# Performance work log

Measured on AMD Instinct MI355X. Metric: run time of the kernel, lower is better.

## Reference

```python
import jax, jax.numpy as jnp
import numpy as np

NS, NV = 64, 32            # multiplicities of irreps_node = 64x0e + 32x1o
D_NODE = NS + 3 * NV       # 160
INV = NS + NV              # 96 invariant features
CUT = 6.0
N_RBF = 32
ZE = 32
EDIM = 16
SQRT3 = 1.7320508075688772


def _mlp3(x, W0, b0, W1, b1, W2, b2):
    h = jax.nn.silu(x @ W0 + b0)
    h = jax.nn.silu(h @ W1 + b1)
    return h @ W2 + b2


def _inv_feats(x):
    # scalars pass through; l=1 blocks -> sqrt(mean over m of x^2 + eps)
    xs = x[..., :NS]
    xv = x[..., NS:].reshape(x.shape[:-1] + (NV, 3))
    return jnp.concatenate([xs, jnp.sqrt(jnp.mean(xv * xv, -1) + 1e-8)], -1)


def _forward(h_full, z, pos, mask, e_feat, z_emb,
             vw_W0, vw_b0, vw_W1, vw_b1, vw_W2, vw_b2,
             sc_W0, sc_b0, sc_W1, sc_b1, sc_W2, sc_b2,
             out_W0, out_b0, out_W1, out_b1, out_W2, out_b2):
    B, N, D = h_full.shape
    dtype = h_full.dtype

    # ---- absorber-relative geometry (absorber_index = 0) ----
    rel = pos - pos[:, :1]                      # (B,N,3)
    r = jnp.sqrt(jnp.sum(rel * rel, -1) + 1e-12)  # (B,N); eps keeps grad finite at absorber
    u = rel / jnp.maximum(r, 1e-8)[..., None]
    valid = mask & (r <= CUT)
    valid = valid.at[:, 0].set(False)

    # ---- invariant features ----
    inv_abs = _inv_feats(h_full[:, 0])          # (B,96)
    inv_nei = _inv_feats(h_full)                # (B,N,96)

    # ---- z embedding + Gaussian RBF(r) ----
    zr = z_emb[z]                               # (B,N,32)
    centers = jnp.linspace(0.0, CUT, N_RBF).astype(dtype)
    delta = CUT / (N_RBF - 1)
    gamma = 1.0 / (delta * delta + 1e-12)
    rc = jnp.minimum(r, CUT)
    rr = jnp.exp(-gamma * (rc[..., None] - centers) ** 2)  # (B,N,32)

    # ---- TP weights from (z_emb, rbf) via 3-layer MLP ----
    vin = jnp.concatenate([zr, rr], -1)         # (B,N,64)
    tp_w = _mlp3(vin, vw_W0, vw_b0, vw_W1, vw_b1, vw_W2, vw_b2)  # (B,N,9216)
    w1 = tp_w[..., :4096].reshape(B, N, NS, NS)        # 0e x 0e -> 0e
    w2 = tp_w[..., 4096:6144].reshape(B, N, NS, NV)    # 0e x 1o -> 1o
    w3 = tp_w[..., 6144:7168].reshape(B, N, NV, NV)    # 1o x 0e -> 1o
    w4 = tp_w[..., 7168:].reshape(B, N, NV, NS)        # 1o x 1o -> 0e

    # ---- FullyConnectedTensorProduct(node, sh) with sh = [1, sqrt(3)*u] ----
    xs = h_full[..., :NS]                        # (B,N,64)
    xv = h_full[..., NS:].reshape(B, N, NV, 3)   # (B,N,32,3)
    y1 = SQRT3 * u                               # component-normalized l=1 SH
    alpha = 1.0 / jnp.sqrt(jnp.asarray(NS + NV, dtype))  # path-normalization
    out_s = alpha * (jnp.einsum('bni,bnio->bno', xs, w1)
                     + jnp.einsum('bnic,bnc,bnio->bno', xv, y1, w4) / SQRT3)
    out_v = alpha * (jnp.einsum('bni,bnio,bnc->bnoc', xs, w2, y1)
                     + jnp.einsum('bnic,bnio->bnoc', xv, w3))
    values = jnp.concatenate([out_s, out_v.reshape(B, N, NV * 3)], -1)  # (B,N,160)

    # ---- score MLP: first layer split by input blocks to avoid the (B,nE,N,272) cat ----
    Wa = sc_W0[:INV]
    Wn = sc_W0[INV:2 * INV]
    Wz = sc_W0[2 * INV:2 * INV + ZE]
    Wr = sc_W0[2 * INV + ZE:2 * INV + ZE + N_RBF]
    We = sc_W0[2 * INV + ZE + N_RBF:]
    pre = ((inv_abs @ Wa)[:, None, None, :]
           + (inv_nei @ Wn + zr @ Wz + rr @ Wr)[:, None, :, :]
           + (e_feat @ We)[None, :, None, :]
           + sc_b0)                              # (B,nE,N,H)
    h1 = jax.nn.silu(pre)
    h2 = jax.nn.silu(h1 @ sc_W1 + sc_b1)
    gate = jax.nn.sigmoid((h2 @ sc_W2 + sc_b2)[..., 0])  # (B,nE,N)

    # ---- cosine cutoff + validity gating ----
    cw = 0.5 * (jnp.cos(jnp.pi * r / CUT) + 1.0) * (r <= CUT).astype(dtype)
    gate = gate * cw[:, None, :] * valid[:, None, :].astype(dtype)

    # ---- normalized gated aggregation over neighbors ----
    agg = jnp.einsum('ben,bnd->bed', gate, values)
    norm = jnp.maximum(jnp.sum(gate, -1, keepdims=True), 1e-8)
    agg = agg / norm                             # (B,nE,160)

    inv_agg = _inv_feats(agg)                    # (B,nE,96)
    return _mlp3(inv_agg, out_W0, out_b0, out_W1, out_b1, out_W2, out_b2)  # (B,nE,128)


def setup_inputs() -> dict:
    key = jax.random.key(0)
    ks = jax.random.split(key, 16)
    B, N, nE, H, LAT = 16, 64, 128, 128, 128
    lin = lambda k, fi, fo: jax.random.normal(k, (fi, fo), jnp.float32) / np.sqrt(fi)
    inp = {
        'h_full': jax.random.normal(ks[0], (B, N, D_NODE), jnp.float32),
        'z': jax.random.randint(ks[1], (B, N), 1, 100),
        'pos': jax.random.normal(ks[2], (B, N, 3), jnp.float32),
        'mask': jnp.ones((B, N), bool),
        'e_feat': jax.random.normal(ks[3], (nE, EDIM), jnp.float32),
        'z_emb': jax.random.normal(ks[4], (101, ZE), jnp.float32),
        'vw_W0': lin(ks[5], ZE + N_RBF, H), 'vw_b0': jnp.zeros((H,), jnp.float32),
        'vw_W1': lin(ks[6], H, H), 'vw_b1': jnp.zeros((H,), jnp.float32),
        'vw_W2': lin(ks[7], H, 9216), 'vw_b2': jnp.zeros((9216,), jnp.float32),
        'sc_W0': lin(ks[8], 2 * INV + ZE + N_RBF + EDIM, H), 'sc_b0': jnp.zeros((H,), jnp.float32),
        'sc_W1': lin(ks[9], H, H), 'sc_b1': jnp.zeros((H,), jnp.float32),
        'sc_W2': lin(ks[10], H, 1), 'sc_b2': jnp.zeros((1,), jnp.float32),
        'out_W0': lin(ks[11], INV, H), 'out_b0': jnp.zeros((H,), jnp.float32),
        'out_W1': lin(ks[12], H, H), 'out_b1': jnp.zeros((H,), jnp.float32),
        'out_W2': lin(ks[13], H, LAT), 'out_b2': jnp.zeros((LAT,), jnp.float32),
    }
    return inp


def reference(h_full, z, pos, mask, e_feat, z_emb,
              vw_W0, vw_b0, vw_W1, vw_b1, vw_W2, vw_b2,
              sc_W0, sc_b0, sc_W1, sc_b1, sc_W2, sc_b2,
              out_W0, out_b0, out_W1, out_b1, out_W2, out_b2):
    return _forward(h_full, z, pos, mask, e_feat, z_emb,
                    vw_W0, vw_b0, vw_W1, vw_b1, vw_W2, vw_b2,
                    sc_W0, sc_b0, sc_W1, sc_b1, sc_W2, sc_b2,
                    out_W0, out_b0, out_W1, out_b1, out_W2, out_b2)
```

## Files before the change

kernel.cpp:

```cpp
#include <hip/hip_runtime.h>
#include <hip/hip_bf16.h>
#include <math.h>

#define SQRT3F 1.7320508075688772f
#define ALPHAF 0.10206207261596577f
#define PIF 3.14159265358979323846f

typedef short v8s __attribute__((ext_vector_type(8)));
typedef float v4f __attribute__((ext_vector_type(4)));

__device__ __forceinline__ float silu_f(float x) {
  return x / (1.0f + __expf(-x));
}
__device__ __forceinline__ float sigmoid_f(float x) {
  return 1.0f / (1.0f + __expf(-x));
}
__device__ __forceinline__ unsigned short f2bf(float f) {
  unsigned int u = __float_as_uint(f);
  unsigned int r = (u + 0x7fffu + ((u >> 16) & 1u)) >> 16;
  return (unsigned short)r;
}
__device__ __forceinline__ float bf2f(unsigned short h) {
  return __uint_as_float(((unsigned int)h) << 16);
}
__device__ __forceinline__ void split_trunc(float x, short* h, short* l) {
  unsigned int u = __float_as_uint(x);
  unsigned short hs = (unsigned short)(u >> 16);
  float r = x - __uint_as_float((unsigned int)hs << 16);
  *h = (short)hs;
  *l = (short)(__float_as_uint(r) >> 16);
}

__device__ __forceinline__ void pack_frag(const float* __restrict__ W, int s0,
                                          unsigned short* __restrict__ fh,
                                          unsigned short* __restrict__ fl) {
  const int lane = s0 & 63;
  const int t = (s0 >> 6) & 7;
  const int ks = s0 >> 9;
  const int kbase = ks * 32 + (lane >> 4) * 8;
  const int n = t * 16 + (lane & 15);
  unsigned short hv[8], lv[8];
  #pragma unroll
  for (int j = 0; j < 8; ++j) {
    float w = W[(size_t)(kbase + j) * 128 + n];
    unsigned short h = f2bf(w);
    hv[j] = h;
    lv[j] = f2bf(w - bf2f(h));
  }
  *(uint4*)&fh[(size_t)s0 * 8] = *(uint4*)hv;
  *(uint4*)&fl[(size_t)s0 * 8] = *(uint4*)lv;
}

__global__ void __launch_bounds__(256) k_front(
    const float* __restrict__ W2, unsigned short* __restrict__ W2fh,
    unsigned short* __restrict__ W2fl,
    const float* __restrict__ hf, const int* __restrict__ z,
    const float* __restrict__ pos, const float* __restrict__ z_emb,
    const float* __restrict__ vwW0, const float* __restrict__ vwb0,
    const float* __restrict__ vwW1, const float* __restrict__ vwb1,
    const float* __restrict__ scW0,
    unsigned short* __restrict__ hTh, unsigned short* __restrict__ hTl,
    float* __restrict__ Pn, float* __restrict__ Pa,
    float* __restrict__ xvu, float* __restrict__ y1cw,
    const float* __restrict__ scW1,
    unsigned short* __restrict__ W1fh, unsigned short* __restrict__ W1fl,
    const float* __restrict__ oW0, const float* __restrict__ oW1,
    const float* __restrict__ oW2,
    unsigned short* __restrict__ O0h, unsigned short* __restrict__ O0l,
    unsigned short* __restrict__ O1h, unsigned short* __restrict__ O1l,
    unsigned short* __restrict__ O2h, unsigned short* __restrict__ O2l,
    const float* __restrict__ e_feat, const float* __restrict__ scb0,
    float* __restrict__ Pe) {
  const int bid = blockIdx.x;
  const int tid = threadIdx.x;
  __shared__ float S[2304];

  if (bid < 576) {
    const int T = bid;
    float (*Tl)[17] = (float(*)[17])S;
    for (int idx = tid; idx < 2048; idx += 256) {
      int k = idx >> 4, cc = idx & 15;
      Tl[k][cc] = W2[(size_t)k * 9216 + T * 16 + cc];
    }
    __syncthreads();
    const int ks = tid >> 6, lane = tid & 63;
    const int q = lane >> 4, cq = lane & 15;
    const int k0 = ks * 32 + q * 8;
    unsigned short hv[8], lv[8];
    #pragma unroll
    for (int j = 0; j < 8; ++j) {
      float wv = Tl[k0 + j][cq];
      unsigned short h = f2bf(wv);
      hv[j] = h;
      lv[j] = f2bf(wv - bf2f(h));
    }
    size_t base = ((size_t)(T * 4 + ks) * 64 + lane) * 8;
    *(uint4*)&W2fh[base] = *(uint4*)hv;
    *(uint4*)&W2fl[base] = *(uint4*)lv;
  } else if (bid < 1088) {
    const int sb = tid >> 7;
    const int t = tid & 127;
    const int g = (bid - 576) * 2 + sb;
    const int b = g >> 6, n = g & 63;
    float* vin  = S + sb * 1152;
    float* invn = vin + 64;
    float* h0   = invn + 96;
    float* uS   = h0 + 128;
    float* rS   = uS + 3;

    if (t == 0) {
      float px = pos[g * 3 + 0] - pos[(b * 64) * 3 + 0];
      float py = pos[g * 3 + 1] - pos[(b * 64) * 3 + 1];
      float pz = pos[g * 3 + 2] - pos[(b * 64) * 3 + 2];
      float r = sqrtf(px * px + py * py + pz * pz + 1e-12f);
      float rm = fmaxf(r, 1e-8f);
      uS[0] = px / rm; uS[1] = py / rm; uS[2] = pz / rm;
      rS[0] = r;
    }
    __syncthreads();
    const float r = rS[0];

    if (t < 32) {
      const float delta = 6.0f / 31.0f;
      const float gamma = 1.0f / (delta * delta + 1e-12f);
      int zi = z[g];
      vin[t] = z_emb[zi * 32 + t];
      float rc = fminf(r, 6.0f);
      float d = rc - (float)t * delta;
      vin[32 + t] = __expf(-gamma * d * d);
      float a = hf[g * 160 + 64 + t * 3 + 0] * uS[0]
              + hf[g * 160 + 64 + t * 3 + 1] * uS[1]
              + hf[g * 160 + 64 + t * 3 + 2] * uS[2];
      xvu[g * 32 + t] = a;
    }
    if (t < 96) {
      if (t < 64) {
        invn[t] = hf[g * 160 + t];
      } else {
        int o = t - 64;
        float v0 = hf[g * 160 + 64 + o * 3 + 0];
        float v1 = hf[g * 160 + 64 + o * 3 + 1];
        float v2 = hf[g * 160 + 64 + o * 3 + 2];
        invn[t] = sqrtf((v0 * v0 + v1 * v1 + v2 * v2) * (1.0f / 3.0f) + 1e-8f);
      }
    }
    if (t == 0) {
      float cw = 0.0f;
      if (r <= 6.0f && n != 0) cw = 0.5f * (cosf(PIF * r * (1.0f / 6.0f)) + 1.0f);
      y1cw[g * 4 + 0] = SQRT3F * uS[0];
      y1cw[g * 4 + 1] = SQRT3F * uS[1];
      y1cw[g * 4 + 2] = SQRT3F * uS[2];
      y1cw[g * 4 + 3] = cw;
    }
    __syncthreads();

    {
      float a = vwb0[t];
      #pragma unroll 8
      for (int k = 0; k < 64; ++k) a = fmaf(vin[k], vwW0[k * 128 + t], a);
      h0[t] = silu_f(a);
    }
    __syncthreads();
    {
      float a = vwb1[t];
      #pragma unroll 8
      for (int k = 0; k < 128; ++k) a = fmaf(h0[k], vwW1[k * 128 + t], a);
      float hv = silu_f(a);
      unsigned short hh = f2bf(hv);
      hTh[(size_t)g * 128 + t] = hh;
      hTl[(size_t)g * 128 + t] = f2bf(hv - bf2f(hh));
    }
    {
      float p = 0.0f;
      #pragma unroll 8
      for (int k = 0; k < 96; ++k) p = fmaf(invn[k], scW0[(96 + k) * 128 + t], p);
      #pragma unroll 8
      for (int k = 0; k < 64; ++k) p = fmaf(vin[k], scW0[(192 + k) * 128 + t], p);
      Pn[(size_t)g * 128 + t] = p;
    }
    if (n == 0) {
      float p = 0.0f;
      #pragma unroll 8
      for (int k = 0; k < 96; ++k) p = fmaf(invn[k], scW0[k * 128 + t], p);
      Pa[b * 128 + t] = p;
    }
  } else {
    const int sb = bid - 1088;
    if (sb < 8) {
      pack_frag(scW1, sb * 256 + tid, W1fh, W1fl);
    } else if (sb < 30) {
      const int s = (sb - 8) * 256 + tid;
      if (s >= 5632) return;
      if (s < 1536)       pack_frag(oW0, s, O0h, O0l);
      else if (s < 3584)  pack_frag(oW1, s - 1536, O1h, O1l);
      else                pack_frag(oW2, s - 3584, O2h, O2l);
    } else {
      const int e = (sb - 30) * 2 + (tid >> 7);
      const int t = tid & 127;
      float a = scb0[t];
      #pragma unroll
      for (int k = 0; k < 16; ++k)
        a = fmaf(e_feat[e * 16 + k], scW0[(256 + k) * 128 + t], a);
      Pe[e * 128 + t] = a;
    }
  }
}

__device__ __forceinline__ int tile_of(int cs, int t) {
  if (t < 8)  return cs * 8 + t;
  if (t < 12) return 256 + cs * 4 + (t - 8);
  if (t < 14) return 384 + cs * 2 + (t - 12);
  return 448 + cs * 4 + (t - 14);
}

__global__ void __launch_bounds__(256) k_tp(
    const unsigned short* __restrict__ hTh, const unsigned short* __restrict__ hTl,
    const unsigned short* __restrict__ W2fh, const unsigned short* __restrict__ W2fl,
    const float* __restrict__ b2, const float* __restrict__ hf,
    const float* __restrict__ xvu, const float* __restrict__ y1cw,
    float* __restrict__ values8) {
  const int bid = blockIdx.x;
  const int cs = bid & 31;
  const int g0 = (bid >> 5) * 64;
  const int p8 = cs & 7;
  const int tid = threadIdx.x;
  const int w = tid >> 6, l = tid & 63;
  const int q = l >> 4, cq = l & 15;

  __shared__ unsigned short BstH[2][256][8];
  __shared__ unsigned short BstL[2][256][8];
  __shared__ float valsS[64][160];
  __shared__ float svS[64][32];

  const int anode = g0 + w * 16 + cq;
  v8s ah0 = *(const v8s*)&hTh[(size_t)anode * 128 + 0 * 32 + q * 8];
  v8s ah1 = *(const v8s*)&hTh[(size_t)anode * 128 + 1 * 32 + q * 8];
  v8s ah2 = *(const v8s*)&hTh[(size_t)anode * 128 + 2 * 32 + q * 8];
  v8s ah3 = *(const v8s*)&hTh[(size_t)anode * 128 + 3 * 32 + q * 8];
  v8s al0 = *(const v8s*)&hTl[(size_t)anode * 128 + 0 * 32 + q * 8];
  v8s al1 = *(const v8s*)&hTl[(size_t)anode * 128 + 1 * 32 + q * 8];
  v8s al2 = *(const v8s*)&hTl[(size_t)anode * 128 + 2 * 32 + q * 8];
  v8s al3 = *(const v8s*)&hTl[(size_t)anode * 128 + 3 * 32 + q * 8];

  float racc1[4][4] = {{0.f}};
  float racc2[2][4] = {{0.f}};
  float racc3[2][4][3] = {{{0.f}}};
  float racc4[4][4] = {{0.f}};

  const int nrow = w * 16 + q * 4;

  {
    const int T = tile_of(cs, 0);
    uint4 gh = *(const uint4*)&W2fh[(size_t)T * 2048 + tid * 8];
    uint4 gl = *(const uint4*)&W2fl[(size_t)T * 2048 + tid * 8];
    *(uint4*)&BstH[0][tid][0] = gh;
    *(uint4*)&BstL[0][tid][0] = gl;
  }
  __syncthreads();

  #pragma unroll
  for (int t = 0; t < 18; ++t) {
    const int buf = t & 1;
    uint4 gh, gl;
    if (t < 17) {
      const int Tn = tile_of(cs, t + 1);
      gh = *(const uint4*)&W2fh[(size_t)Tn * 2048 + tid * 8];
      gl = *(const uint4*)&W2fl[(size_t)Tn * 2048 + tid * 8];
    }

    const int T = tile_of(cs, t);
    v8s bh0 = *(const v8s*)&BstH[buf][0 * 64 + l][0];
    v8s bh1 = *(const v8s*)&BstH[buf][1 * 64 + l][0];
    v8s bh2 = *(const v8s*)&BstH[buf][2 * 64 + l][0];
    v8s bh3 = *(const v8s*)&BstH[buf][3 * 64 + l][0];
    v8s bl0 = *(const v8s*)&BstL[buf][0 * 64 + l][0];
    v8s bl1 = *(const v8s*)&BstL[buf][1 * 64 + l][0];
    v8s bl2 = *(const v8s*)&BstL[buf][2 * 64 + l][0];
    v8s bl3 = *(const v8s*)&BstL[buf][3 * 64 + l][0];

    v4f a0 = (v4f){0.f, 0.f, 0.f, 0.f};
    v4f a1 = (v4f){0.f, 0.f, 0.f, 0.f};
    v4f a2 = (v4f){0.f, 0.f, 0.f, 0.f};
    a0 = __builtin_amdgcn_mfma_f32_16x16x32_bf16(ah0, bh0, a0, 0, 0, 0);
    a1 = __builtin_amdgcn_mfma_f32_16x16x32_bf16(al0, bh0, a1, 0, 0, 0);
    a2 = __builtin_amdgcn_mfma_f32_16x16x32_bf16(ah0, bl0, a2, 0, 0, 0);
    a0 = __builtin_amdgcn_mfma_f32_16x16x32_bf16(ah1, bh1, a0, 0, 0, 0);
    a1 = __builtin_amdgcn_mfma_f32_16x16x32_bf16(al1, bh1, a1, 0, 0, 0);
    a2 = __builtin_amdgcn_mfma_f32_16x16x32_bf16(ah1, bl1, a2, 0, 0, 0);
    a0 = __builtin_amdgcn_mfma_f32_16x16x32_bf16(ah2, bh2, a0, 0, 0, 0);
    a1 = __builtin_amdgcn_mfma_f32_16x16x32_bf16(al2, bh2, a1, 0, 0, 0);
    a2 = __builtin_amdgcn_mfma_f32_16x16x32_bf16(ah2, bl2, a2, 0, 0, 0);
    a0 = __builtin_amdgcn_mfma_f32_16x16x32_bf16(ah3, bh3, a0, 0, 0, 0);
    a1 = __builtin_amdgcn_mfma_f32_16x16x32_bf16(al3, bh3, a1, 0, 0, 0);
    a2 = __builtin_amdgcn_mfma_f32_16x16x32_bf16(ah3, bl3, a2, 0, 0, 0);
    a0 += a1; a0 += a2;
    const float bj = b2[T * 16 + cq];
    v4f tp = a0;
    tp[0] += bj; tp[1] += bj; tp[2] += bj; tp[3] += bj;

    if (t < 8) {
      const int i = cs * 2 + (t >> 2);
      const int m = t & 3;
      #pragma unroll
      for (int r = 0; r < 4; ++r)
        racc1[m][r] = fmaf(hf[(size_t)(g0 + nrow + r) * 160 + i], tp[r], racc1[m][r]);
    } else if (t < 12) {
      const int i = cs * 2 + ((t - 8) >> 1);
      const int m = (t - 8) & 1;
      #pragma unroll
      for (int r = 0; r < 4; ++r)
        racc2[m][r] = fmaf(hf[(size_t)(g0 + nrow + r) * 160 + i], tp[r], racc2[m][r]);
    } else if (t < 14) {
      const int m = (t - 12) & 1;
      #pragma unroll
      for (int r = 0; r < 4; ++r) {
        const float* xvp = hf + (size_t)(g0 + nrow + r) * 160 + 64 + 3 * cs;
        #pragma unroll
        for (int cc = 0; cc < 3; ++cc)
          racc3[m][r][cc] = fmaf(xvp[cc], tp[r], racc3[m][r][cc]);
      }
    } else {
      const int m = (t - 14) & 3;
      #pragma unroll
      for (int r = 0; r < 4; ++r)
        racc4[m][r] = fmaf(xvu[(size_t)(g0 + nrow + r) * 32 + cs], tp[r], racc4[m][r]);
    }

    if (t < 17) {
      const int nbuf = buf ^ 1;
      *(uint4*)&BstH[nbuf][tid][0] = gh;
      *(uint4*)&BstL[nbuf][tid][0] = gl;
    }
    __syncthreads();
  }

  #pragma unroll
  for (int r = 0; r < 4; ++r) {
    const int n = nrow + r;
    #pragma unroll
    for (int m = 0; m < 4; ++m)
      valsS[n][m * 16 + cq] = racc1[m][r] + racc4[m][r];
    #pragma unroll
    for (int m = 0; m < 2; ++m)
      svS[n][m * 16 + cq] = racc2[m][r];
    #pragma unroll
    for (int m = 0; m < 2; ++m)
      #pragma unroll
      for (int cc = 0; cc < 3; ++cc)
        valsS[n][64 + 3 * (m * 16 + cq) + cc] = racc3[m][r][cc];
  }
  __syncthreads();

  float* vtgt = values8 + (size_t)p8 * 163840;
  const float* y1b = y1cw + (size_t)g0 * 4;
  for (int idx = tid; idx < 10240; idx += 256) {
    int n = idx / 160, d = idx - n * 160;
    float v = valsS[n][d];
    if (d >= 64) {
      int dd = d - 64, o = dd / 3, cc = dd - 3 * o;
      v = fmaf(svS[n][o], y1b[n * 4 + cc], v);
    }
    atomicAdd(&vtgt[(size_t)(g0 + n) * 160 + d], v);
  }
}

__global__ void __launch_bounds__(256) k_reduce(
    const float* __restrict__ values8, float* __restrict__ values) {
  const int s = blockIdx.x * 256 + threadIdx.x;
  float4 acc = make_float4(0.f, 0.f, 0.f, 0.f);
  #pragma unroll
  for (int p = 0; p < 8; ++p) {
    float4 v = *(const float4*)&values8[(size_t)p * 163840 + s * 4];
    acc.x += v.x; acc.y += v.y; acc.z += v.z; acc.w += v.w;
  }
  acc.x *= ALPHAF; acc.y *= ALPHAF; acc.z *= ALPHAF; acc.w *= ALPHAF;
  *(float4*)&values[(size_t)s * 4] = acc;
}

__global__ void __launch_bounds__(256, 4) k_gate(
    const float* __restrict__ Pa, const float* __restrict__ Pe,
    const float* __restrict__ Pn,
    const unsigned short* __restrict__ W1fh, const unsigned short* __restrict__ W1fl,
    const float* __restrict__ b1, const float* __restrict__ W2v,
    const float* __restrict__ b2s, const float* __restrict__ y1cw,
    float* __restrict__ gate) {
  const int bid = blockIdx.x;
  const int b = bid >> 6;
  const int e0 = (bid & 63) * 2, e1 = e0 + 1;
  const int tid = threadIdx.x;

  __shared__ float Prow0[128], Prow1[128];
  __shared__ float gpre[2][64];

  if (tid < 128) {
    float pa = Pa[b * 128 + tid];
    Prow0[tid] = pa + Pe[e0 * 128 + tid];
    Prow1[tid] = pa + Pe[e1 * 128 + tid];
  }
  __syncthreads();

  const int w = tid >> 6, l = tid & 63;
  const int q = l >> 4, cq = l & 15;
  const int node = w * 16 + cq;
  const float* pnrow = Pn + (size_t)(b * 64 + node) * 128;

  v4f acc0[8], acc1[8];
  #pragma unroll
  for (int t = 0; t < 8; ++t) {
    acc0[t] = (v4f){0.f, 0.f, 0.f, 0.f};
    acc1[t] = (v4f){0.f, 0.f, 0.f, 0.f};
  }

  #pragma unroll
  for (int ks = 0; ks < 4; ++ks) {
    const int k0 = ks * 32 + q * 8;
    float4 p0 = *(const float4*)(pnrow + k0);
    float4 p1 = *(const float4*)(pnrow + k0 + 4);
    float pv[8] = {p0.x, p0.y, p0.z, p0.w, p1.x, p1.y, p1.z, p1.w};
    float4 r00 = *(const float4*)(&Prow0[k0]);
    float4 r01 = *(const float4*)(&Prow0[k0 + 4]);
    float4 r10 = *(const float4*)(&Prow1[k0]);
    float4 r11 = *(const float4*)(&Prow1[k0 + 4]);
    float rv0[8] = {r00.x, r00.y, r00.z, r00.w, r01.x, r01.y, r01.z, r01.w};
    float rv1[8] = {r10.x, r10.y, r10.z, r10.w, r11.x, r11.y, r11.z, r11.w};
    v8s a0h, a0l, a1h, a1l;
    #pragma unroll
    for (int j = 0; j < 8; ++j) {
      short hs, ls;
      split_trunc(silu_f(pv[j] + rv0[j]), &hs, &ls);
      a0h[j] = hs; a0l[j] = ls;
      split_trunc(silu_f(pv[j] + rv1[j]), &hs, &ls);
      a1h[j] = hs; a1l[j] = ls;
    }
    #pragma unroll
    for (int t = 0; t < 8; ++t) {
      const size_t fb = (size_t)((ks * 8 + t) * 64 + l) * 8;
      v8s bh = *(const v8s*)&W1fh[fb];
      v8s bl = *(const v8s*)&W1fl[fb];
      acc0[t] = __builtin_amdgcn_mfma_f32_16x16x32_bf16(a0h, bh, acc0[t], 0, 0, 0);
      acc0[t] = __builtin_amdgcn_mfma_f32_16x16x32_bf16(a0l, bh, acc0[t], 0, 0, 0);
      acc0[t] = __builtin_amdgcn_mfma_f32_16x16x32_bf16(a0h, bl, acc0[t], 0, 0, 0);
      acc1[t] = __builtin_amdgcn_mfma_f32_16x16x32_bf16(a1h, bh, acc1[t], 0, 0, 0);
      acc1[t] = __builtin_amdgcn_mfma_f32_16x16x32_bf16(a1l, bh, acc1[t], 0, 0, 0);
      acc1[t] = __builtin_amdgcn_mfma_f32_16x16x32_bf16(a1h, bl, acc1[t], 0, 0, 0);
    }
  }

  float p00 = 0.f, p01 = 0.f, p02 = 0.f, p03 = 0.f;
  float p10 = 0.f, p11 = 0.f, p12 = 0.f, p13 = 0.f;
  #pragma unroll
  for (int t = 0; t < 8; ++t) {
    float bb = b1[t * 16 + cq];
    float wg = W2v[t * 16 + cq];
    p00 = fmaf(silu_f(acc0[t][0] + bb), wg, p00);
    p01 = fmaf(silu_f(acc0[t][1] + bb), wg, p01);
    p02 = fmaf(silu_f(acc0[t][2] + bb), wg, p02);
    p03 = fmaf(silu_f(acc0[t][3] + bb), wg, p03);
    p10 = fmaf(silu_f(acc1[t][0] + bb), wg, p10);
    p11 = fmaf(silu_f(acc1[t][1] + bb), wg, p11);
    p12 = fmaf(silu_f(acc1[t][2] + bb), wg, p12);
    p13 = fmaf(silu_f(acc1[t][3] + bb), wg, p13);
  }
  #pragma unroll
  for (int off = 1; off < 16; off <<= 1) {
    p00 += __shfl_xor(p00, off); p01 += __shfl_xor(p01, off);
    p02 += __shfl_xor(p02, off); p03 += __shfl_xor(p03, off);
    p10 += __shfl_xor(p10, off); p11 += __shfl_xor(p11, off);
    p12 += __shfl_xor(p12, off); p13 += __shfl_xor(p13, off);
  }
  if (cq == 0) {
    gpre[0][w * 16 + q * 4 + 0] = p00;
    gpre[0][w * 16 + q * 4 + 1] = p01;
    gpre[0][w * 16 + q * 4 + 2] = p02;
    gpre[0][w * 16 + q * 4 + 3] = p03;
    gpre[1][w * 16 + q * 4 + 0] = p10;
    gpre[1][w * 16 + q * 4 + 1] = p11;
    gpre[1][w * 16 + q * 4 + 2] = p12;
    gpre[1][w * 16 + q * 4 + 3] = p13;
  }
  __syncthreads();

  if (tid < 128) {
    const int ee = tid >> 6, ll = tid & 63;
    float gv = sigmoid_f(gpre[ee][ll] + b2s[0]);
    gv *= y1cw[(b * 64 + ll) * 4 + 3];
    float t2 = gv;
    #pragma unroll
    for (int off = 32; off > 0; off >>= 1) t2 += __shfl_xor(t2, off);
    float inv = 1.0f / fmaxf(t2, 1e-8f);
    const int e = (ee == 0) ? e0 : e1;
    gate[(size_t)(b * 128 + e) * 64 + ll] = gv * inv;
  }
}

__global__ void __launch_bounds__(256) k_out(
    const float* __restrict__ gate, const float* __restrict__ values,
    const unsigned short* __restrict__ O0h, const unsigned short* __restrict__ O0l,
    const unsigned short* __restrict__ O1h, const unsigned short* __restrict__ O1l,
    const unsigned short* __restrict__ O2h, const unsigned short* __restrict__ O2l,
    const float* __restrict__ b0, const float* __restrict__ b1,
    const float* __restrict__ b2, float* __restrict__ out) {
  const int r0 = blockIdx.x * 16;
  const int bb_ = r0 >> 7;
  const int tid = threadIdx.x;
  const int w = tid >> 6, l = tid & 63;
  const int q = l >> 4, cq = l & 15;
  const int t0 = 2 * w, t1 = 2 * w + 1;

  __shared__ float SH[13824];
  float* vSf = SH;
  float* gSf = SH + 10240;
  float* aSf = SH + 11264;
  float* xSf = SH;
  float (*hS)[132] = (float(*)[132])(SH + 2048);

  {
    const float4* src = (const float4*)(values + (size_t)bb_ * 10240);
    float4* dst = (float4*)vSf;
    for (int i = tid; i < 2560; i += 256) dst[i] = src[i];
    ((float4*)gSf)[tid] = ((const float4*)(gate + (size_t)r0 * 64))[tid];
  }
  __syncthreads();

  #pragma unroll
  for (int it = 0; it < 5; ++it) {
    const int idx = it * 256 + tid;
    const int row = idx / 80;
    const int d = (idx - row * 80) * 2;
    const float* gr = gSf + row * 64;
    float ax = 0.f, ay = 0.f;
    #pragma unroll 4
    for (int n = 0; n < 64; ++n) {
      float g = gr[n];
      float2 v = *(const float2*)&vSf[n * 160 + d];
      ax = fmaf(g, v.x, ax);
      ay = fmaf(g, v.y, ay);
    }
    aSf[row * 160 + d]     = ax;
    aSf[row * 160 + d + 1] = ay;
  }
  __syncthreads();

  for (int idx = tid; idx < 1536; idx += 256) {
    const int row = idx / 96;
    const int ll = idx - row * 96;
    float rv;
    if (ll < 64) {
      rv = aSf[row * 160 + ll];
    } else {
      const int o = ll - 64;
      float a0 = aSf[row * 160 + 64 + 3 * o + 0];
      float a1 = aSf[row * 160 + 64 + 3 * o + 1];
      float a2 = aSf[row * 160 + 64 + 3 * o + 2];
      rv = sqrtf((a0 * a0 + a1 * a1 + a2 * a2) * (1.0f / 3.0f) + 1e-8f);
    }
    xSf[row * 104 + ll] = rv;
  }
  __syncthreads();

  v4f acc0 = (v4f){0.f, 0.f, 0.f, 0.f};
  v4f acc1 = (v4f){0.f, 0.f, 0.f, 0.f};
  {
    const float* xrow = xSf + cq * 104 + q * 8;
    #pragma unroll
    for (int ks = 0; ks < 3; ++ks) {
      float4 p0 = *(const float4*)(xrow + ks * 32);
      float4 p1 = *(const float4*)(xrow + ks * 32 + 4);
      float xv[8] = {p0.x, p0.y, p0.z, p0.w, p1.x, p1.y, p1.z, p1.w};
      v8s avh, avl;
      #pragma unroll
      for (int j = 0; j < 8; ++j) {
        short hs, ls;
        split_trunc(xv[j], &hs, &ls);
        avh[j] = hs; avl[j] = ls;
      }
      v8s b0h = *(const v8s*)&O0h[((size_t)(ks * 8 + t0) * 64 + l) * 8];
      v8s b0l = *(const v8s*)&O0l[((size_t)(ks * 8 + t0) * 64 + l) * 8];
      v8s b1h = *(const v8s*)&O0h[((size_t)(ks * 8 + t1) * 64 + l) * 8];
      v8s b1l = *(const v8s*)&O0l[((size_t)(ks * 8 + t1) * 64 + l) * 8];
      acc0 = __builtin_amdgcn_mfma_f32_16x16x32_bf16(avh, b0h, acc0, 0, 0, 0);
      acc0 = __builtin_amdgcn_mfma_f32_16x16x32_bf16(avl, b0h, acc0, 0, 0, 0);
      acc0 = __builtin_amdgcn_mfma_f32_16x16x32_bf16(avh, b0l, acc0, 0, 0, 0);
      acc1 = __builtin_amdgcn_mfma_f32_16x16x32_bf16(avh, b1h, acc1, 0, 0, 0);
      acc1 = __builtin_amdgcn_mfma_f32_16x16x32_bf16(avl, b1h, acc1, 0, 0, 0);
      acc1 = __builtin_amdgcn_mfma_f32_16x16x32_bf16(avh, b1l, acc1, 0, 0, 0);
    }
  }
  __syncthreads();
  {
    const float bb0 = b0[t0 * 16 + cq], bb1 = b0[t1 * 16 + cq];
    #pragma unroll
    for (int r = 0; r < 4; ++r) {
      hS[q * 4 + r][t0 * 16 + cq] = silu_f(acc0[r] + bb0);
      hS[q * 4 + r][t1 * 16 + cq] = silu_f(acc1[r] + bb1);
    }
  }
  __syncthreads();

  v8s a2h[4], a2l[4];
  #pragma unroll
  for (int ks = 0; ks < 4; ++ks) {
    float4 p0 = *(const float4*)&hS[cq][ks * 32 + q * 8];
    float4 p1 = *(const float4*)&hS[cq][ks * 32 + q * 8 + 4];
    float xv[8] = {p0.x, p0.y, p0.z, p0.w, p1.x, p1.y, p1.z, p1.w};
    #pragma unroll
    for (int j = 0; j < 8; ++j) {
      short hs, ls;
      split_trunc(xv[j], &hs, &ls);
      a2h[ks][j] = hs; a2l[ks][j] = ls;
    }
  }
  __syncthreads();
  acc0 = (v4f){0.f, 0.f, 0.f, 0.f};
  acc1 = (v4f){0.f, 0.f, 0.f, 0.f};
  #pragma unroll
  for (int ks = 0; ks < 4; ++ks) {
    v8s b0h = *(const v8s*)&O1h[((size_t)(ks * 8 + t0) * 64 + l) * 8];
    v8s b0l = *(const v8s*)&O1l[((size_t)(ks * 8 + t0) * 64 + l) * 8];
    v8s b1h = *(const v8s*)&O1h[((size_t)(ks * 8 + t1) * 64 + l) * 8];
    v8s b1l = *(const v8s*)&O1l[((size_t)(ks * 8 + t1) * 64 + l) * 8];
    acc0 = __builtin_amdgcn_mfma_f32_16x16x32_bf16(a2h[ks], b0h, acc0, 0, 0, 0);
    acc0 = __builtin_amdgcn_mfma_f32_16x16x32_bf16(a2l[ks], b0h, acc0, 0, 0, 0);
    acc0 = __builtin_amdgcn_mfma_f32_16x16x32_bf16(a2h[ks], b0l, acc0, 0, 0, 0);
    acc1 = __builtin_amdgcn_mfma_f32_16x16x32_bf16(a2h[ks], b1h, acc1, 0, 0, 0);
    acc1 = __builtin_amdgcn_mfma_f32_16x16x32_bf16(a2l[ks], b1h, acc1, 0, 0, 0);
    acc1 = __builtin_amdgcn_mfma_f32_16x16x32_bf16(a2h[ks], b1l, acc1, 0, 0, 0);
  }
  {
    const float bb0 = b1[t0 * 16 + cq], bb1 = b1[t1 * 16 + cq];
    #pragma unroll
    for (int r = 0; r < 4; ++r) {
      hS[q * 4 + r][t0 * 16 + cq] = silu_f(acc0[r] + bb0);
      hS[q * 4 + r][t1 * 16 + cq] = silu_f(acc1[r] + bb1);
    }
  }
  __syncthreads();

  #pragma unroll
  for (int ks = 0; ks < 4; ++ks) {
    float4 p0 = *(const float4*)&hS[cq][ks * 32 + q * 8];
    float4 p1 = *(const float4*)&hS[cq][ks * 32 + q * 8 + 4];
    float xv[8] = {p0.x, p0.y, p0.z, p0.w, p1.x, p1.y, p1.z, p1.w};
    #pragma unroll
    for (int j = 0; j < 8; ++j) {
      short hs, ls;
      split_trunc(xv[j], &hs, &ls);
      a2h[ks][j] = hs; a2l[ks][j] = ls;
    }
  }
  acc0 = (v4f){0.f, 0.f, 0.f, 0.f};
  acc1 = (v4f){0.f, 0.f, 0.f, 0.f};
  #pragma unroll
  for (int ks = 0; ks < 4; ++ks) {
    v8s b0h = *(const v8s*)&O2h[((size_t)(ks * 8 + t0) * 64 + l) * 8];
    v8s b0l = *(const v8s*)&O2l[((size_t)(ks * 8 + t0) * 64 + l) * 8];
    v8s b1h = *(const v8s*)&O2h[((size_t)(ks * 8 + t1) * 64 + l) * 8];
    v8s b1l = *(const v8s*)&O2l[((size_t)(ks * 8 + t1) * 64 + l) * 8];
    acc0 = __builtin_amdgcn_mfma_f32_16x16x32_bf16(a2h[ks], b0h, acc0, 0, 0, 0);
    acc0 = __builtin_amdgcn_mfma_f32_16x16x32_bf16(a2l[ks], b0h, acc0, 0, 0, 0);
    acc0 = __builtin_amdgcn_mfma_f32_16x16x32_bf16(a2h[ks], b0l, acc0, 0, 0, 0);
    acc1 = __builtin_amdgcn_mfma_f32_16x16x32_bf16(a2h[ks], b1h, acc1, 0, 0, 0);
    acc1 = __builtin_amdgcn_mfma_f32_16x16x32_bf16(a2l[ks], b1h, acc1, 0, 0, 0);
    acc1 = __builtin_amdgcn_mfma_f32_16x16x32_bf16(a2h[ks], b1l, acc1, 0, 0, 0);
  }
  {
    const float bb0 = b2[t0 * 16 + cq], bb1 = b2[t1 * 16 + cq];
    #pragma unroll
    for (int r = 0; r < 4; ++r) {
      out[(size_t)(r0 + q * 4 + r) * 128 + t0 * 16 + cq] = acc0[r] + bb0;
      out[(size_t)(r0 + q * 4 + r) * 128 + t1 * 16 + cq] = acc1[r] + bb1;
    }
  }
}

extern "C" void kernel_launch(void* const* d_in, const int* in_sizes, int n_in,
                              void* d_out, int out_size, void* d_ws, size_t ws_size,
                              hipStream_t stream) {
  const float* hf    = (const float*)d_in[0];
  const int*   z     = (const int*)  d_in[1];
  const float* pos   = (const float*)d_in[2];
  const float* e_feat= (const float*)d_in[4];
  const float* z_emb = (const float*)d_in[5];
  const float* vwW0  = (const float*)d_in[6];
  const float* vwb0  = (const float*)d_in[7];
  const float* vwW1  = (const float*)d_in[8];
  const float* vwb1  = (const float*)d_in[9];
  const float* vwW2  = (const float*)d_in[10];
  const float* vwb2  = (const float*)d_in[11];
  const float* scW0  = (const float*)d_in[12];
  const float* scb0  = (const float*)d_in[13];
  const float* scW1  = (const float*)d_in[14];
  const float* scb1  = (const float*)d_in[15];
  const float* scW2  = (const float*)d_in[16];
  const float* scb2  = (const float*)d_in[17];
  const float* oW0   = (const float*)d_in[18];
  const float* ob0   = (const float*)d_in[19];
  const float* oW1   = (const float*)d_in[20];
  const float* ob1   = (const float*)d_in[21];
  const float* oW2   = (const float*)d_in[22];
  const float* ob2   = (const float*)d_in[23];
  float* out = (float*)d_out;

  float* ws = (float*)d_ws;
  unsigned short* W2fh = (unsigned short*)(ws);
  unsigned short* W2fl = (unsigned short*)(ws + 589824);
  unsigned short* hTh  = (unsigned short*)(ws + 1179648);
  unsigned short* hTl  = (unsigned short*)(ws + 1245184);
  float* Pn     = ws + 1310720;
  float* Pa     = Pn + 131072;
  float* Pe     = Pa + 2048;
  float* xvu    = Pe + 16384;
  float* y1cw   = xvu + 32768;
  float* values = y1cw + 4096;
  float* gate   = values + 163840;
  unsigned short* W1fh = (unsigned short*)(gate + 196608);
  unsigned short* W1fl = (unsigned short*)(gate + 196608 + 8192);
  float* values8 = gate + 196608 + 16384;
  unsigned short* Ob = (unsigned short*)(values8 + 8 * 163840);
  unsigned short* O0h = Ob;
  unsigned short* O0l = Ob + 12288;
  unsigned short* O1h = Ob + 24576;
  unsigned short* O1l = Ob + 40960;
  unsigned short* O2h = Ob + 57344;
  unsigned short* O2l = Ob + 73728;

  hipMemsetAsync(values8, 0, 8 * 163840 * sizeof(float), stream);

  k_front<<<1182, 256, 0, stream>>>(
      vwW2, W2fh, W2fl,
      hf, z, pos, z_emb, vwW0, vwb0, vwW1, vwb1, scW0,
      hTh, hTl, Pn, Pa, xvu, y1cw,
      scW1, W1fh, W1fl, oW0, oW1, oW2,
      O0h, O0l, O1h, O1l, O2h, O2l,
      e_feat, scb0, Pe);
  k_tp<<<512, 256, 0, stream>>>(hTh, hTl, W2fh, W2fl, vwb2, hf, xvu,
                                y1cw, values8);
  k_reduce<<<160, 256, 0, stream>>>(values8, values);
  k_gate<<<1024, 256, 0, stream>>>(Pa, Pe, Pn, W1fh, W1fl, scb1, scW2, scb2,
                                   y1cw, gate);
  k_out<<<128, 256, 0, stream>>>(gate, values, O0h, O0l, O1h, O1l, O2h, O2l,
                                 ob0, ob1, ob2, out);
}
```

Baseline: 206.9 us.

## Split tensor-product kernel into two halves and move aggregation into separate kernel

The tensor-product kernel's 18-tile loop is split into two templated halves (tiles 0-7 and 8-17), and the grid doubles to 1024 blocks. The goal is more parallelism and shorter per-block serial chains. Node features and biases are hoisted into registers, and the staged shared-memory epilogue is replaced by direct per-thread atomic adds. The gate-weighted aggregation and invariant-feature step move out of k_out into a new k_agg kernel with 256 blocks, which raises parallelism but adds one launch and a global round-trip for the aggregated features.

```diff
diff --git a/kernel.cpp b/kernel.cpp
--- a/kernel.cpp
+++ b/kernel.cpp
@@ -213,24 +213,19 @@
   return 448 + cs * 4 + (t - 14);
 }
 
-__global__ void __launch_bounds__(256) k_tp(
+template <int TB, int TN>
+__device__ __forceinline__ void tp_body(
+    unsigned short (* __restrict__ BstH)[256][8],
+    unsigned short (* __restrict__ BstL)[256][8],
     const unsigned short* __restrict__ hTh, const unsigned short* __restrict__ hTl,
     const unsigned short* __restrict__ W2fh, const unsigned short* __restrict__ W2fl,
     const float* __restrict__ b2, const float* __restrict__ hf,
     const float* __restrict__ xvu, const float* __restrict__ y1cw,
-    float* __restrict__ values8) {
-  const int bid = blockIdx.x;
-  const int cs = bid & 31;
-  const int g0 = (bid >> 5) * 64;
-  const int p8 = cs & 7;
+    float* __restrict__ values8, int cs, int g0, int p8) {
   const int tid = threadIdx.x;
   const int w = tid >> 6, l = tid & 63;
   const int q = l >> 4, cq = l & 15;
-
-  __shared__ unsigned short BstH[2][256][8];
-  __shared__ unsigned short BstL[2][256][8];
-  __shared__ float valsS[64][160];
-  __shared__ float svS[64][32];
+  const int nrow = w * 16 + q * 4;
 
   const int anode = g0 + w * 16 + cq;
   v8s ah0 = *(const v8s*)&hTh[(size_t)anode * 128 + 0 * 32 + q * 8];
@@ -242,15 +237,30 @@
   v8s al2 = *(const v8s*)&hTl[(size_t)anode * 128 + 2 * 32 + q * 8];
   v8s al3 = *(const v8s*)&hTl[(size_t)anode * 128 + 3 * 32 + q * 8];
 
+  float hfa[2][4], hfv3[4][3], xv4[4];
+  #pragma unroll
+  for (int r = 0; r < 4; ++r) {
+    const float* hrow = hf + (size_t)(g0 + nrow + r) * 160;
+    hfa[0][r] = hrow[cs * 2];
+    hfa[1][r] = hrow[cs * 2 + 1];
+    if (TB != 0) {
+      hfv3[r][0] = hrow[64 + 3 * cs + 0];
+      hfv3[r][1] = hrow[64 + 3 * cs + 1];
+      hfv3[r][2] = hrow[64 + 3 * cs + 2];
+      xv4[r] = xvu[(size_t)(g0 + nrow + r) * 32 + cs];
+    }
+  }
+  float bjv[TN];
+  #pragma unroll
+  for (int j = 0; j < TN; ++j) bjv[j] = b2[tile_of(cs, TB + j) * 16 + cq];
+
   float racc1[4][4] = {{0.f}};
   float racc2[2][4] = {{0.f}};
   float racc3[2][4][3] = {{{0.f}}};
   float racc4[4][4] = {{0.f}};
 
-  const int nrow = w * 16 + q * 4;
-
   {
-    const int T = tile_of(cs, 0);
+    const int T = tile_of(cs, TB);
     uint4 gh = *(const uint4*)&W2fh[(size_t)T * 2048 + tid * 8];
     uint4 gl = *(const uint4*)&W2fl[(size_t)T * 2048 + tid * 8];
     *(uint4*)&BstH[0][tid][0] = gh;
@@ -259,16 +269,16 @@
   __syncthreads();
 
   #pragma unroll
-  for (int t = 0; t < 18; ++t) {
-    const int buf = t & 1;
+  for (int j = 0; j < TN; ++j) {
+    const int buf = j & 1;
+    const int t = TB + j;
     uint4 gh, gl;
-    if (t < 17) {
+    if (j < TN - 1) {
       const int Tn = tile_of(cs, t + 1);
       gh = *(const uint4*)&W2fh[(size_t)Tn * 2048 + tid * 8];
       gl = *(const uint4*)&W2fl[(size_t)Tn * 2048 + tid * 8];
     }
 
-    const int T = tile_of(cs, t);
     v8s bh0 = *(const v8s*)&BstH[buf][0 * 64 + l][0];
     v8s bh1 = *(const v8s*)&BstH[buf][1 * 64 + l][0];
     v8s bh2 = *(const v8s*)&BstH[buf][2 * 64 + l][0];
@@ -294,39 +304,37 @@
     a1 = __builtin_amdgcn_mfma_f32_16x16x32_bf16(al3, bh3, a1, 0, 0, 0);
     a2 = __builtin_amdgcn_mfma_f32_16x16x32_bf16(ah3, bl3, a2, 0, 0, 0);
     a0 += a1; a0 += a2;
-    const float bj = b2[T * 16 + cq];
+    const float bj = bjv[j];
     v4f tp = a0;
     tp[0] += bj; tp[1] += bj; tp[2] += bj; tp[3] += bj;
 
     if (t < 8) {
-      const int i = cs * 2 + (t >> 2);
+      const int ii = t >> 2;
       const int m = t & 3;
       #pragma unroll
       for (int r = 0; r < 4; ++r)
-        racc1[m][r] = fmaf(hf[(size_t)(g0 + nrow + r) * 160 + i], tp[r], racc1[m][r]);
+        racc1[m][r] = fmaf(hfa[ii][r], tp[r], racc1[m][r]);
     } else if (t < 12) {
-      const int i = cs * 2 + ((t - 8) >> 1);
+      const int ii = (t - 8) >> 1;
       const int m = (t - 8) & 1;
       #pragma unroll
       for (int r = 0; r < 4; ++r)
-        racc2[m][r] = fmaf(hf[(size_t)(g0 + nrow + r) * 160 + i], tp[r], racc2[m][r]);
+        racc2[m][r] = fmaf(hfa[ii][r], tp[r], racc2[m][r]);
     } else if (t < 14) {
       const int m = (t - 12) & 1;
       #pragma unroll
-      for (int r = 0; r < 4; ++r) {
-        const float* xvp = hf + (size_t)(g0 + nrow + r) * 160 + 64 + 3 * cs;
+      for (int r = 0; r < 4; ++r)
         #pragma unroll
         for (int cc = 0; cc < 3; ++cc)
-          racc3[m][r][cc] = fmaf(xvp[cc], tp[r], racc3[m][r][cc]);
-      }
+          racc3[m][r][cc] = fmaf(hfv3[r][cc], tp[r], racc3[m][r][cc]);
     } else {
       const int m = (t - 14) & 3;
       #pragma unroll
       for (int r = 0; r < 4; ++r)
-        racc4[m][r] = fmaf(xvu[(size_t)(g0 + nrow + r) * 32 + cs], tp[r], racc4[m][r]);
-    }
-
-    if (t < 17) {
+        racc4[m][r] = fmaf(xv4[r], tp[r], racc4[m][r]);
+    }
+
+    if (j < TN - 1) {
       const int nbuf = buf ^ 1;
       *(uint4*)&BstH[nbuf][tid][0] = gh;
       *(uint4*)&BstL[nbuf][tid][0] = gl;
@@ -334,34 +342,54 @@
     __syncthreads();
   }
 
+  float* vtgt = values8 + (size_t)p8 * 163840;
   #pragma unroll
   for (int r = 0; r < 4; ++r) {
     const int n = nrow + r;
-    #pragma unroll
-    for (int m = 0; m < 4; ++m)
-      valsS[n][m * 16 + cq] = racc1[m][r] + racc4[m][r];
-    #pragma unroll
-    for (int m = 0; m < 2; ++m)
-      svS[n][m * 16 + cq] = racc2[m][r];
-    #pragma unroll
-    for (int m = 0; m < 2; ++m)
-      #pragma unroll
-      for (int cc = 0; cc < 3; ++cc)
-        valsS[n][64 + 3 * (m * 16 + cq) + cc] = racc3[m][r][cc];
-  }
-  __syncthreads();
-
-  float* vtgt = values8 + (size_t)p8 * 163840;
-  const float* y1b = y1cw + (size_t)g0 * 4;
-  for (int idx = tid; idx < 10240; idx += 256) {
-    int n = idx / 160, d = idx - n * 160;
-    float v = valsS[n][d];
-    if (d >= 64) {
-      int dd = d - 64, o = dd / 3, cc = dd - 3 * o;
-      v = fmaf(svS[n][o], y1b[n * 4 + cc], v);
-    }
-    atomicAdd(&vtgt[(size_t)(g0 + n) * 160 + d], v);
-  }
+    float* vrow = vtgt + (size_t)(g0 + n) * 160;
+    if (TB == 0) {
+      #pragma unroll
+      for (int m = 0; m < 4; ++m)
+        atomicAdd(&vrow[m * 16 + cq], racc1[m][r]);
+    } else {
+      float4 y1v = *(const float4*)&y1cw[(size_t)(g0 + n) * 4];
+      float y1a[3] = {y1v.x, y1v.y, y1v.z};
+      #pragma unroll
+      for (int m = 0; m < 4; ++m)
+        atomicAdd(&vrow[m * 16 + cq], racc4[m][r]);
+      #pragma unroll
+      for (int m = 0; m < 2; ++m) {
+        const int o = m * 16 + cq;
+        #pragma unroll
+        for (int cc = 0; cc < 3; ++cc)
+          atomicAdd(&vrow[64 + 3 * o + cc],
+                    racc3[m][r][cc] + racc2[m][r] * y1a[cc]);
+      }
+    }
+  }
+}
+
+__global__ void __launch_bounds__(256) k_tp(
+    const unsigned short* __restrict__ hTh, const unsigned short* __restrict__ hTl,
+    const unsigned short* __restrict__ W2fh, const unsigned short* __restrict__ W2fl,
+    const float* __restrict__ b2, const float* __restrict__ hf,
+    const float* __restrict__ xvu, const float* __restrict__ y1cw,
+    float* __restrict__ values8) {
+  const int bid = blockIdx.x;
+  const int cs = bid & 31;
+  const int g0 = ((bid >> 5) & 15) * 64;
+  const int half = bid >> 9;
+  const int p8 = cs & 7;
+
+  __shared__ unsigned short BstH[2][256][8];
+  __shared__ unsigned short BstL[2][256][8];
+
+  if (half == 0)
+    tp_body<0, 8>(BstH, BstL, hTh, hTl, W2fh, W2fl, b2, hf, xvu, y1cw,
+                  values8, cs, g0, p8);
+  else
+    tp_body<8, 10>(BstH, BstL, hTh, hTl, W2fh, W2fl, b2, hf, xvu, y1cw,
+                   values8, cs, g0, p8);
 }
 
 __global__ void __launch_bounds__(256) k_reduce(
@@ -493,75 +521,78 @@
   }
 }
 
+__global__ void __launch_bounds__(256) k_agg(
+    const float* __restrict__ gate, const float* __restrict__ values,
+    float* __restrict__ inv_agg) {
+  const int bid = blockIdx.x;
+  const int b = bid >> 4;
+  const int eg = bid & 15;
+  const int tid = threadIdx.x;
+
+  __shared__ float vS[10240];
+  __shared__ float gS[8][64];
+  __shared__ float aS[8][160];
+
+  {
+    const float4* src = (const float4*)(values + (size_t)b * 10240);
+    float4* dst = (float4*)vS;
+    #pragma unroll
+    for (int i = 0; i < 10; ++i) dst[tid + i * 256] = src[tid + i * 256];
+    if (tid < 128)
+      ((float4*)gS)[tid] =
+          ((const float4*)(gate + ((size_t)b * 128 + eg * 8) * 64))[tid];
+  }
+  __syncthreads();
+
+  #pragma unroll
+  for (int it = 0; it < 5; ++it) {
+    const int idx = it * 256 + tid;
+    const int row = idx / 160;
+    const int d = idx - row * 160;
+    const float* gr = &gS[row][0];
+    float a = 0.f;
+    #pragma unroll 8
+    for (int n = 0; n < 64; ++n) a = fmaf(gr[n], vS[n * 160 + d], a);
+    aS[row][d] = a;
+  }
+  __syncthreads();
+
+  for (int idx = tid; idx < 768; idx += 256) {
+    const int row = idx / 96;
+    const int ll = idx - row * 96;
+    float rv;
+    if (ll < 64) {
+      rv = aS[row][ll];
+    } else {
+      const int o = ll - 64;
+      float a0 = aS[row][64 + 3 * o + 0];
+      float a1 = aS[row][64 + 3 * o + 1];
+      float a2 = aS[row][64 + 3 * o + 2];
+      rv = sqrtf((a0 * a0 + a1 * a1 + a2 * a2) * (1.0f / 3.0f) + 1e-8f);
+    }
+    inv_agg[((size_t)b * 128 + eg * 8 + row) * 96 + ll] = rv;
+  }
+}
+
 __global__ void __launch_bounds__(256) k_out(
-    const float* __restrict__ gate, const float* __restrict__ values,
+    const float* __restrict__ X,
     const unsigned short* __restrict__ O0h, const unsigned short* __restrict__ O0l,
     const unsigned short* __restrict__ O1h, const unsigned short* __restrict__ O1l,
     const unsigned short* __restrict__ O2h, const unsigned short* __restrict__ O2l,
     const float* __restrict__ b0, const float* __restrict__ b1,
     const float* __restrict__ b2, float* __restrict__ out) {
   const int r0 = blockIdx.x * 16;
-  const int bb_ = r0 >> 7;
   const int tid = threadIdx.x;
   const int w = tid >> 6, l = tid & 63;
   const int q = l >> 4, cq = l & 15;
   const int t0 = 2 * w, t1 = 2 * w + 1;
 
-  __shared__ float SH[13824];
-  float* vSf = SH;
-  float* gSf = SH + 10240;
-  float* aSf = SH + 11264;
-  float* xSf = SH;
-  float (*hS)[132] = (float(*)[132])(SH + 2048);
-
-  {
-    const float4* src = (const float4*)(values + (size_t)bb_ * 10240);
-    float4* dst = (float4*)vSf;
-    for (int i = tid; i < 2560; i += 256) dst[i] = src[i];
-    ((float4*)gSf)[tid] = ((const float4*)(gate + (size_t)r0 * 64))[tid];
-  }
-  __syncthreads();
-
-  #pragma unroll
-  for (int it = 0; it < 5; ++it) {
-    const int idx = it * 256 + tid;
-    const int row = idx / 80;
-    const int d = (idx - row * 80) * 2;
-    const float* gr = gSf + row * 64;
-    float ax = 0.f, ay = 0.f;
-    #pragma unroll 4
-    for (int n = 0; n < 64; ++n) {
-      float g = gr[n];
-      float2 v = *(const float2*)&vSf[n * 160 + d];
-      ax = fmaf(g, v.x, ax);
-      ay = fmaf(g, v.y, ay);
-    }
-    aSf[row * 160 + d]     = ax;
-    aSf[row * 160 + d + 1] = ay;
-  }
-  __syncthreads();
-
-  for (int idx = tid; idx < 1536; idx += 256) {
-    const int row = idx / 96;
-    const int ll = idx - row * 96;
-    float rv;
-    if (ll < 64) {
-      rv = aSf[row * 160 + ll];
-    } else {
-      const int o = ll - 64;
-      float a0 = aSf[row * 160 + 64 + 3 * o + 0];
-      float a1 = aSf[row * 160 + 64 + 3 * o + 1];
-      float a2 = aSf[row * 160 + 64 + 3 * o + 2];
-      rv = sqrtf((a0 * a0 + a1 * a1 + a2 * a2) * (1.0f / 3.0f) + 1e-8f);
-    }
-    xSf[row * 104 + ll] = rv;
-  }
-  __syncthreads();
+  __shared__ float hS[16][132];
 
   v4f acc0 = (v4f){0.f, 0.f, 0.f, 0.f};
   v4f acc1 = (v4f){0.f, 0.f, 0.f, 0.f};
   {
-    const float* xrow = xSf + cq * 104 + q * 8;
+    const float* xrow = X + (size_t)(r0 + cq) * 96 + q * 8;
     #pragma unroll
     for (int ks = 0; ks < 3; ++ks) {
       float4 p0 = *(const float4*)(xrow + ks * 32);
@@ -586,7 +617,6 @@
       acc1 = __builtin_amdgcn_mfma_f32_16x16x32_bf16(avh, b1l, acc1, 0, 0, 0);
     }
   }
-  __syncthreads();
   {
     const float bb0 = b0[t0 * 16 + cq], bb1 = b0[t1 * 16 + cq];
     #pragma unroll
@@ -723,6 +753,7 @@
   unsigned short* O1l = Ob + 40960;
   unsigned short* O2h = Ob + 57344;
   unsigned short* O2l = Ob + 73728;
+  float* invagg = (float*)(Ob + 90112);
 
   hipMemsetAsync(values8, 0, 8 * 163840 * sizeof(float), stream);
 
@@ -733,11 +764,12 @@
       scW1, W1fh, W1fl, oW0, oW1, oW2,
       O0h, O0l, O1h, O1l, O2h, O2l,
       e_feat, scb0, Pe);
-  k_tp<<<512, 256, 0, stream>>>(hTh, hTl, W2fh, W2fl, vwb2, hf, xvu,
-                                y1cw, values8);
+  k_tp<<<1024, 256, 0, stream>>>(hTh, hTl, W2fh, W2fl, vwb2, hf, xvu,
+                                 y1cw, values8);
   k_reduce<<<160, 256, 0, stream>>>(values8, values);
   k_gate<<<1024, 256, 0, stream>>>(Pa, Pe, Pn, W1fh, W1fl, scb1, scW2, scb2,
                                    y1cw, gate);
-  k_out<<<128, 256, 0, stream>>>(gate, values, O0h, O0l, O1h, O1l, O2h, O2l,
+  k_agg<<<256, 256, 0, stream>>>(gate, values, invagg);
+  k_out<<<128, 256, 0, stream>>>(invagg, O0h, O0l, O1h, O1l, O2h, O2l,
                                  ob0, ob1, ob2, out);
 }
```

Result: slower. 230.9 us (+11.6%).

## Use async global-to-LDS loads in k_tp and split aggregation out of k_out

Applied to the files above, without the earlier changes.

The double-buffered weight-tile staging in k_tp now uses global_load_lds to copy straight into shared memory, dropping the register round-trip and the deferred store after compute. The gated aggregation and invariant-feature step moves out of k_out into a new k_agg kernel. k_agg launches 256 blocks of 8 edges each, so the aggregation is spread over more blocks. k_out then reads the precomputed features from global memory, at the cost of one extra launch and a global write/read of the intermediate.

```diff
diff --git a/kernel.cpp b/kernel.cpp
--- a/kernel.cpp
+++ b/kernel.cpp
@@ -29,6 +29,13 @@
   float r = x - __uint_as_float((unsigned int)hs << 16);
   *h = (short)hs;
   *l = (short)(__float_as_uint(r) >> 16);
+}
+
+__device__ __forceinline__ void async_lds16(const unsigned short* __restrict__ g,
+                                            unsigned short* l) {
+  __builtin_amdgcn_global_load_lds(
+      (const __attribute__((address_space(1))) unsigned int*)g,
+      (__attribute__((address_space(3))) unsigned int*)l, 16, 0, 0);
 }
 
 __device__ __forceinline__ void pack_frag(const float* __restrict__ W, int s0,
@@ -251,21 +258,18 @@
 
   {
     const int T = tile_of(cs, 0);
-    uint4 gh = *(const uint4*)&W2fh[(size_t)T * 2048 + tid * 8];
-    uint4 gl = *(const uint4*)&W2fl[(size_t)T * 2048 + tid * 8];
-    *(uint4*)&BstH[0][tid][0] = gh;
-    *(uint4*)&BstL[0][tid][0] = gl;
+    async_lds16(&W2fh[(size_t)T * 2048 + tid * 8], &BstH[0][tid][0]);
+    async_lds16(&W2fl[(size_t)T * 2048 + tid * 8], &BstL[0][tid][0]);
   }
   __syncthreads();
 
   #pragma unroll
   for (int t = 0; t < 18; ++t) {
     const int buf = t & 1;
-    uint4 gh, gl;
     if (t < 17) {
       const int Tn = tile_of(cs, t + 1);
-      gh = *(const uint4*)&W2fh[(size_t)Tn * 2048 + tid * 8];
-      gl = *(const uint4*)&W2fl[(size_t)Tn * 2048 + tid * 8];
+      async_lds16(&W2fh[(size_t)Tn * 2048 + tid * 8], &BstH[buf ^ 1][tid][0]);
+      async_lds16(&W2fl[(size_t)Tn * 2048 + tid * 8], &BstL[buf ^ 1][tid][0]);
     }
 
     const int T = tile_of(cs, t);
@@ -325,12 +329,6 @@
       for (int r = 0; r < 4; ++r)
         racc4[m][r] = fmaf(xvu[(size_t)(g0 + nrow + r) * 32 + cs], tp[r], racc4[m][r]);
     }
-
-    if (t < 17) {
-      const int nbuf = buf ^ 1;
-      *(uint4*)&BstH[nbuf][tid][0] = gh;
-      *(uint4*)&BstL[nbuf][tid][0] = gl;
-    }
     __syncthreads();
   }
 
@@ -493,75 +491,78 @@
   }
 }
 
+__global__ void __launch_bounds__(256) k_agg(
+    const float* __restrict__ gate, const float* __restrict__ values,
+    float* __restrict__ inv_agg) {
+  const int bid = blockIdx.x;
+  const int b = bid >> 4;
+  const int eg = bid & 15;
+  const int tid = threadIdx.x;
+
+  __shared__ float vS[10240];
+  __shared__ float gS[8][64];
+  __shared__ float aS[8][160];
+
+  {
+    const float4* src = (const float4*)(values + (size_t)b * 10240);
+    float4* dst = (float4*)vS;
+    #pragma unroll
+    for (int i = 0; i < 10; ++i) dst[tid + i * 256] = src[tid + i * 256];
+    if (tid < 128)
+      ((float4*)gS)[tid] =
+          ((const float4*)(gate + ((size_t)b * 128 + eg * 8) * 64))[tid];
+  }
+  __syncthreads();
+
+  #pragma unroll
+  for (int it = 0; it < 5; ++it) {
+    const int idx = it * 256 + tid;
+    const int row = idx / 160;
+    const int d = idx - row * 160;
+    const float* gr = &gS[row][0];
+    float a = 0.f;
+    #pragma unroll 8
+    for (int n = 0; n < 64; ++n) a = fmaf(gr[n], vS[n * 160 + d], a);
+    aS[row][d] = a;
+  }
+  __syncthreads();
+
+  for (int idx = tid; idx < 768; idx += 256) {
+    const int row = idx / 96;
+    const int ll = idx - row * 96;
+    float rv;
+    if (ll < 64) {
+      rv = aS[row][ll];
+    } else {
+      const int o = ll - 64;
+      float a0 = aS[row][64 + 3 * o + 0];
+      float a1 = aS[row][64 + 3 * o + 1];
+      float a2 = aS[row][64 + 3 * o + 2];
+      rv = sqrtf((a0 * a0 + a1 * a1 + a2 * a2) * (1.0f / 3.0f) + 1e-8f);
+    }
+    inv_agg[((size_t)b * 128 + eg * 8 + row) * 96 + ll] = rv;
+  }
+}
+
 __global__ void __launch_bounds__(256) k_out(
-    const float* __restrict__ gate, const float* __restrict__ values,
+    const float* __restrict__ X,
     const unsigned short* __restrict__ O0h, const unsigned short* __restrict__ O0l,
     const unsigned short* __restrict__ O1h, const unsigned short* __restrict__ O1l,
     const unsigned short* __restrict__ O2h, const unsigned short* __restrict__ O2l,
     const float* __restrict__ b0, const float* __restrict__ b1,
     const float* __restrict__ b2, float* __restrict__ out) {
   const int r0 = blockIdx.x * 16;
-  const int bb_ = r0 >> 7;
   const int tid = threadIdx.x;
   const int w = tid >> 6, l = tid & 63;
   const int q = l >> 4, cq = l & 15;
   const int t0 = 2 * w, t1 = 2 * w + 1;
 
-  __shared__ float SH[13824];
-  float* vSf = SH;
-  float* gSf = SH + 10240;
-  float* aSf = SH + 11264;
-  float* xSf = SH;
-  float (*hS)[132] = (float(*)[132])(SH + 2048);
-
-  {
-    const float4* src = (const float4*)(values + (size_t)bb_ * 10240);
-    float4* dst = (float4*)vSf;
-    for (int i = tid; i < 2560; i += 256) dst[i] = src[i];
-    ((float4*)gSf)[tid] = ((const float4*)(gate + (size_t)r0 * 64))[tid];
-  }
-  __syncthreads();
-
-  #pragma unroll
-  for (int it = 0; it < 5; ++it) {
-    const int idx = it * 256 + tid;
-    const int row = idx / 80;
-    const int d = (idx - row * 80) * 2;
-    const float* gr = gSf + row * 64;
-    float ax = 0.f, ay = 0.f;
-    #pragma unroll 4
-    for (int n = 0; n < 64; ++n) {
-      float g = gr[n];
-      float2 v = *(const float2*)&vSf[n * 160 + d];
-      ax = fmaf(g, v.x, ax);
-      ay = fmaf(g, v.y, ay);
-    }
-    aSf[row * 160 + d]     = ax;
-    aSf[row * 160 + d + 1] = ay;
-  }
-  __syncthreads();
-
-  for (int idx = tid; idx < 1536; idx += 256) {
-    const int row = idx / 96;
-    const int ll = idx - row * 96;
-    float rv;
-    if (ll < 64) {
-      rv = aSf[row * 160 + ll];
-    } else {
-      const int o = ll - 64;
-      float a0 = aSf[row * 160 + 64 + 3 * o + 0];
-      float a1 = aSf[row * 160 + 64 + 3 * o + 1];
-      float a2 = aSf[row * 160 + 64 + 3 * o + 2];
-      rv = sqrtf((a0 * a0 + a1 * a1 + a2 * a2) * (1.0f / 3.0f) + 1e-8f);
-    }
-    xSf[row * 104 + ll] = rv;
-  }
-  __syncthreads();
+  __shared__ float hS[16][132];
 
   v4f acc0 = (v4f){0.f, 0.f, 0.f, 0.f};
   v4f acc1 = (v4f){0.f, 0.f, 0.f, 0.f};
   {
-    const float* xrow = xSf + cq * 104 + q * 8;
+    const float* xrow = X + (size_t)(r0 + cq) * 96 + q * 8;
     #pragma unroll
     for (int ks = 0; ks < 3; ++ks) {
       float4 p0 = *(const float4*)(xrow + ks * 32);
@@ -586,7 +587,6 @@
       acc1 = __builtin_amdgcn_mfma_f32_16x16x32_bf16(avh, b1l, acc1, 0, 0, 0);
     }
   }
-  __syncthreads();
   {
     const float bb0 = b0[t0 * 16 + cq], bb1 = b0[t1 * 16 + cq];
     #pragma unroll
@@ -723,6 +723,7 @@
   unsigned short* O1l = Ob + 40960;
   unsigned short* O2h = Ob + 57344;
   unsigned short* O2l = Ob + 73728;
+  float* invagg = (float*)(Ob + 90112);
 
   hipMemsetAsync(values8, 0, 8 * 163840 * sizeof(float), stream);
 
@@ -738,6 +739,7 @@
   k_reduce<<<160, 256, 0, stream>>>(values8, values);
   k_gate<<<1024, 256, 0, stream>>>(Pa, Pe, Pn, W1fh, W1fl, scb1, scW2, scb2,
                                    y1cw, gate);
-  k_out<<<128, 256, 0, stream>>>(gate, values, O0h, O0l, O1h, O1l, O2h, O2l,
+  k_agg<<<256, 256, 0, stream>>>(gate, values, invagg);
+  k_out<<<128, 256, 0, stream>>>(invagg, O0h, O0l, O1h, O1l, O2h, O2l,
                                  ob0, ob1, ob2, out);
 }
```

After: 204.7 us. No clear change (-1.0%).
